# Performance work log

Hardware: AMD Instinct MI355X
Metric: run time of the kernel (lower is better)

The kernel has to match this reference:

```python
import jax, jax.numpy as jnp
import numpy as np

DIM = 256  # channel width
B, H, W = 4, 64, 64


def conv2d(x, w, b, pad, groups=1):
    # x: NCHW, w: OIHW (I = C_in/groups)
    y = jax.lax.conv_general_dilated(
        x, w, window_strides=(1, 1),
        padding=[(pad[0], pad[0]), (pad[1], pad[1])],
        dimension_numbers=("NCHW", "OIHW", "NCHW"),
        feature_group_count=groups)
    return y + b[None, :, None, None]


def l2norm(x, eps=1e-12):
    # matches F.normalize(x, dim=-1): x / max(||x||_2, eps)
    n = jnp.sqrt(jnp.sum(x * x, axis=-1, keepdims=True))
    return x / jnp.maximum(n, eps)


def setup_inputs() -> dict:
    key = jax.random.key(0)
    ks = jax.random.split(key, 12)
    dim, c8 = DIM, DIM // 8
    w = lambda k, shape, s: jax.random.normal(k, shape, jnp.float32) * s
    return {
        "x": jax.random.normal(ks[0], (B, dim, H, W), jnp.float32),
        "w_conv": w(ks[1], (dim, dim, 3, 3), 0.02), "b_conv": jnp.zeros((dim,), jnp.float32),
        "w01": w(ks[2], (dim, 1, 1, 7), 0.05), "b01": jnp.zeros((dim,), jnp.float32),
        "w02": w(ks[3], (dim, 1, 7, 1), 0.05), "b02": jnp.zeros((dim,), jnp.float32),
        "w11": w(ks[4], (dim, 1, 1, 11), 0.05), "b11": jnp.zeros((dim,), jnp.float32),
        "w12": w(ks[5], (dim, 1, 11, 1), 0.05), "b12": jnp.zeros((dim,), jnp.float32),
        "w21": w(ks[6], (dim, 1, 1, 21), 0.05), "b21": jnp.zeros((dim,), jnp.float32),
        "w22": w(ks[7], (dim, 1, 21, 1), 0.05), "b22": jnp.zeros((dim,), jnp.float32),
        "w_proj": w(ks[8], (c8, dim, 1, 1), 0.05), "b_proj": jnp.zeros((c8,), jnp.float32),
        "w3": w(ks[9], (c8, dim // 4, 1, 1), 0.05), "b3": jnp.zeros((c8,), jnp.float32),
        "w4": w(ks[10], (dim, c8, 1, 1), 0.05), "b4": jnp.zeros((dim,), jnp.float32),
    }


def reference(x, w_conv, b_conv, w01, b01, w02, b02, w11, b11, w12, b12,
              w21, b21, w22, b22, w_proj, b_proj, w3, b3, w4, b4):
    b, c, h, w_ = x.shape
    x = conv2d(x, w_conv, b_conv, (1, 1))
    # multi-scale separable depthwise convs (7, 11, 21)
    x1 = conv2d(conv2d(x, w01, b01, (0, 3), c), w02, b02, (3, 0), c)
    x2 = conv2d(conv2d(x, w11, b11, (0, 5), c), w12, b12, (5, 0), c)
    x3 = conv2d(conv2d(x, w21, b21, (0, 10), c), w22, b22, (10, 0), c)
    out1 = x1 + x2 + x3 + x                      # [b, dim, h, w]
    out1 = conv2d(out1, w_proj, b_proj, (0, 0))  # [b, dim//8, h, w]
    c8 = out1.shape[1]
    t = out1.reshape(b, c8, h * w_)              # b head c (h w), head=1

    q1 = l2norm(t)
    attn1 = jax.nn.softmax(q1 @ jnp.swapaxes(q1, -2, -1), axis=-1)  # [b, c8, c8]
    out2 = attn1 @ t                                                # [b, c8, hw]

    # branch 2: spatial attention (hw x hw)
    ts = jnp.swapaxes(t, -2, -1)                 # [b, hw, c8]
    q2 = l2norm(ts)
    attn2 = jax.nn.softmax(q2 @ jnp.swapaxes(q2, -2, -1), axis=-1)  # [b, hw, hw]
    out3 = jnp.swapaxes(attn2 @ ts, -2, -1)                         # [b, c8, hw]

    out4 = jnp.concatenate([out2.reshape(b, c8, h, w_),
                            out3.reshape(b, c8, h, w_)], axis=1)    # [b, dim//4, h, w]
    out5 = conv2d(out4, w3, b3, (0, 0)) + out1
    return conv2d(out5, w4, b4, (0, 0))          # [b, dim, h, w]
```

## Files before the change

### kernel.cpp

```cpp
#include <hip/hip_runtime.h>
#include <hip/hip_bf16.h>

typedef __hip_bfloat16 bf16;
typedef short s16;
typedef __attribute__((ext_vector_type(4))) short s16x4;
typedef __attribute__((ext_vector_type(8))) short s16x8;
typedef __attribute__((ext_vector_type(4))) float f32x4;

__device__ __forceinline__ s16 f2b(float f){
    unsigned u = __float_as_uint(f);
    unsigned r = (u + 0x7FFFu + ((u >> 16) & 1u)) >> 16;
    return (s16)r;
}
__device__ __forceinline__ float b2f_bits(s16 v){
    return __uint_as_float(((unsigned)(unsigned short)v) << 16);
}

__global__ __launch_bounds__(256) void xtrans_k(const float* __restrict__ x, s16* __restrict__ xcl){
    __shared__ s16 lb[64][258];
    int h = blockIdx.x, b = blockIdx.y, t = threadIdx.x;
    for (int i = t; i < 16384; i += 256){
        int ci = i >> 6, w = i & 63;
        lb[w][ci] = f2b(x[((b*256 + ci)*64 + h)*64 + w]);
    }
    __syncthreads();
    for (int i = t; i < 16384; i += 256){
        int w = i >> 8, ci = i & 255;
        xcl[(b*4096 + h*64 + w)*256 + ci] = lb[w][ci];
    }
}

__global__ __launch_bounds__(256) void wpack_k(const float* __restrict__ w, s16* __restrict__ wpk){
    int idx = blockIdx.x*256 + threadIdx.x;
    int cil = idx & 31;
    int r   = idx >> 5;
    int co  = r & 255;
    int r2  = r >> 8;
    int tap = r2 % 9, cc = r2 / 9;
    wpk[idx] = f2b(w[(co*256 + cc*32 + cil)*9 + tap]);
}

__global__ __launch_bounds__(256) void conv3x3m_k(const s16* __restrict__ xcl,
        const s16* __restrict__ wpk, const float* __restrict__ bias,
        bf16* __restrict__ y0){
    __shared__ alignas(16) s16 smem[30240];
    s16* xls = smem;
    s16* wls = smem + 9504;
    const int sp = blockIdx.x, cog = blockIdx.y;
    const int b = sp >> 5, h0 = (sp & 31)*2;
    const int t = threadIdx.x;
    const int wv = t >> 6, lane = t & 63;
    const int lm = lane & 15, g = lane >> 4;

    f32x4 acc[2][4];
    #pragma unroll
    for (int mi = 0; mi < 2; ++mi)
        #pragma unroll
        for (int ni = 0; ni < 4; ++ni) acc[mi][ni] = (f32x4){0.f,0.f,0.f,0.f};

    for (int cc = 0; cc < 8; ++cc){
        __syncthreads();
        for (int i = t; i < 1056; i += 256){
            int g8 = i & 3, wi = (i>>2) % 66, r = (i>>2) / 66;
            int h = h0 - 1 + r, w = wi - 1;
            s16x8 v = {0,0,0,0,0,0,0,0};
            if (h >= 0 && h < 64 && w >= 0 && w < 64)
                v = *(const s16x8*)&xcl[(b*4096 + h*64 + w)*256 + cc*32 + g8*8];
            s16* d = &xls[(r*66 + wi)*36 + g8*8];
            *(s16x4*)d       = __builtin_shufflevector(v, v, 0,1,2,3);
            *(s16x4*)(d + 4) = __builtin_shufflevector(v, v, 4,5,6,7);
        }
        for (int i = t; i < 2304; i += 256){
            int g8 = i & 3, co = (i>>2) & 63, tap = i >> 8;
            s16x8 v = *(const s16x8*)&wpk[((cc*9 + tap)*256 + cog*64 + co)*32 + g8*8];
            s16* d = &wls[(tap*64 + co)*36 + g8*8];
            *(s16x4*)d       = __builtin_shufflevector(v, v, 0,1,2,3);
            *(s16x4*)(d + 4) = __builtin_shufflevector(v, v, 4,5,6,7);
        }
        __syncthreads();
        #pragma unroll
        for (int tap = 0; tap < 9; ++tap){
            const int kh = tap/3, kw = tap%3;
            s16x8 bfr[4], afr[2];
            #pragma unroll
            for (int ni = 0; ni < 4; ++ni){
                const s16* p = &wls[(tap*64 + ni*16 + lm)*36 + g*8];
                s16x4 lo = *(const s16x4*)p;
                s16x4 hi = *(const s16x4*)(p + 4);
                bfr[ni] = __builtin_shufflevector(lo, hi, 0,1,2,3,4,5,6,7);
            }
            #pragma unroll
            for (int mi = 0; mi < 2; ++mi){
                int m = (wv*2 + mi)*16 + lm;
                int hr = m >> 6, ww = m & 63;
                const s16* p = &xls[((hr + kh)*66 + (ww + kw))*36 + g*8];
                s16x4 lo = *(const s16x4*)p;
                s16x4 hi = *(const s16x4*)(p + 4);
                afr[mi] = __builtin_shufflevector(lo, hi, 0,1,2,3,4,5,6,7);
            }
            #pragma unroll
            for (int mi = 0; mi < 2; ++mi)
                #pragma unroll
                for (int ni = 0; ni < 4; ++ni)
                    acc[mi][ni] = __builtin_amdgcn_mfma_f32_16x16x32_bf16(
                        afr[mi], bfr[ni], acc[mi][ni], 0, 0, 0);
        }
    }
    __syncthreads();
    float* ot = (float*)smem;
    #pragma unroll
    for (int mi = 0; mi < 2; ++mi)
        #pragma unroll
        for (int ni = 0; ni < 4; ++ni)
            #pragma unroll
            for (int r = 0; r < 4; ++r){
                int m  = (wv*2 + mi)*16 + g*4 + r;
                int co = ni*16 + lm;
                ot[co*132 + m] = acc[mi][ni][r];
            }
    __syncthreads();
    for (int i = t; i < 8192; i += 256){
        int co = i >> 7, m = i & 127;
        float v = ot[co*132 + m] + bias[cog*64 + co];
        y0[((b*256 + cog*64 + co)*64 + h0 + (m>>6))*64 + (m & 63)] = __float2bfloat16(v);
    }
}

template<int K>
__device__ __forceinline__ void sep_branch(const float (*__restrict__ pl)[65], float (*__restrict__ hp)[65],
                                           int c, int t,
                                           const float* __restrict__ wh, const float* __restrict__ bh,
                                           const float* __restrict__ wv, const float* __restrict__ bv,
                                           float* acc){
    constexpr int P = K/2;
    constexpr int W = 16 + 2*P;
    float wk[K];
    #pragma unroll
    for (int j = 0; j < K; ++j) wk[j] = wh[c*K + j];
    float bhv = bh[c];
    {
        int h = t >> 2, w0 = (t & 3)*16;
        float win[W];
        #pragma unroll
        for (int j = 0; j < W; ++j){
            int ww = w0 - P + j;
            win[j] = (ww >= 0 && ww < 64) ? pl[h][ww] : 0.f;
        }
        __syncthreads();
        #pragma unroll
        for (int i = 0; i < 16; ++i){
            float s = bhv;
            #pragma unroll
            for (int k = 0; k < K; ++k) s += win[i+k]*wk[k];
            hp[h][w0 + i] = s;
        }
    }
    float vk[K];
    #pragma unroll
    for (int j = 0; j < K; ++j) vk[j] = wv[c*K + j];
    float bvv = bv[c];
    __syncthreads();
    {
        int w = t & 63, h0 = (t >> 6)*16;
        float win[W];
        #pragma unroll
        for (int j = 0; j < W; ++j){
            int hh = h0 - P + j;
            win[j] = (hh >= 0 && hh < 64) ? hp[hh][w] : 0.f;
        }
        #pragma unroll
        for (int i = 0; i < 16; ++i){
            float s = bvv;
            #pragma unroll
            for (int k = 0; k < K; ++k) s += win[i+k]*vk[k];
            acc[i] += s;
        }
    }
}

__global__ __launch_bounds__(256) void sepconv_k(const bf16* __restrict__ y0,
        const float* __restrict__ w01, const float* __restrict__ b01,
        const float* __restrict__ w02, const float* __restrict__ b02,
        const float* __restrict__ w11, const float* __restrict__ b11,
        const float* __restrict__ w12, const float* __restrict__ b12,
        const float* __restrict__ w21, const float* __restrict__ b21,
        const float* __restrict__ w22, const float* __restrict__ b22,
        bf16* __restrict__ out1){
    __shared__ float pl[64][65];
    __shared__ float hp[64][65];
    int bc = blockIdx.x;
    int c = bc & 255;
    int t = threadIdx.x;
    const bf16* src = y0 + bc*4096;
    for (int i = t; i < 4096; i += 256) pl[i>>6][i&63] = __bfloat162float(src[i]);
    __syncthreads();
    float acc[16];
    #pragma unroll
    for (int k = 0; k < 16; ++k) acc[k] = 0.f;
    sep_branch<7 >(pl, hp, c, t, w01, b01, w02, b02, acc);
    sep_branch<11>(pl, hp, c, t, w11, b11, w12, b12, acc);
    sep_branch<21>(pl, hp, c, t, w21, b21, w22, b22, acc);
    bf16* dst = out1 + bc*4096;
    {
        int w = t & 63, h0 = (t >> 6)*16;
        #pragma unroll
        for (int i = 0; i < 16; ++i)
            dst[(h0 + i)*64 + w] = __float2bfloat16(acc[i] + pl[h0 + i][w]);
    }
}

__global__ __launch_bounds__(256) void proj_k(const bf16* __restrict__ out1, const float* __restrict__ wp,
                                              const float* __restrict__ bp, float* __restrict__ tbuf,
                                              s16* __restrict__ tTb, float* __restrict__ rn2){
    __shared__ float wl[256*32];
    __shared__ s16 part[4][64][36];
    int pt = blockIdx.x, b = blockIdx.y, t = threadIdx.x;
    int q = t >> 6, lane = t & 63;
    for (int i = t; i < 8192; i += 256){
        int ci = i >> 5, cc = i & 31;
        wl[ci*32 + cc] = wp[cc*256 + ci];
    }
    __syncthreads();
    int p = pt*64 + lane;
    float acc[32] = {};
    const bf16* xb = out1 + b*1048576 + p;
    for (int ci = q*64; ci < q*64 + 64; ++ci){
        float v = __bfloat162float(xb[ci*4096]);
        const float* wr = &wl[ci*32];
        #pragma unroll
        for (int c8 = 0; c8 < 8; ++c8){
            float4 w4 = *(const float4*)&wr[c8*4];
            acc[c8*4+0] += w4.x*v; acc[c8*4+1] += w4.y*v;
            acc[c8*4+2] += w4.z*v; acc[c8*4+3] += w4.w*v;
        }
    }
    #pragma unroll
    for (int cc = 0; cc < 32; ++cc) part[q][lane][cc] = f2b(acc[cc]);
    __syncthreads();
    int p_loc = t >> 2, qq = t & 3;
    int pg = pt*64 + p_loc;
    float a8[8];
    float ss = 0.f;
    #pragma unroll
    for (int c = 0; c < 8; ++c){
        int cc = qq*8 + c;
        float v = b2f_bits(part[0][p_loc][cc]) + b2f_bits(part[1][p_loc][cc])
                + b2f_bits(part[2][p_loc][cc]) + b2f_bits(part[3][p_loc][cc]) + bp[cc];
        a8[c] = v;
        ss += v*v;
    }
    ss += __shfl_xor(ss, 1, 4);
    ss += __shfl_xor(ss, 2, 4);
    if (qq == 0) rn2[b*4096 + pg] = 1.f / fmaxf(sqrtf(ss), 1e-12f);
    #pragma unroll
    for (int c = 0; c < 8; ++c) tbuf[(b*32 + qq*8 + c)*4096 + pg] = a8[c];
    s16x8 o8;
    #pragma unroll
    for (int c = 0; c < 8; ++c) o8[c] = f2b(a8[c]);
    *(s16x8*)&tTb[(b*4096 + pg)*32 + qq*8] = o8;
}

__global__ __launch_bounds__(256) void gramm_k(const float* __restrict__ tbuf, float* __restrict__ part){
    __shared__ alignas(16) s16 ts[32*268];
    int ks = blockIdx.x, b = blockIdx.y, t = threadIdx.x;
    {
        int cc = t >> 3, p0 = (t & 7)*32;
        const float* src = tbuf + (b*32 + cc)*4096 + ks*256 + p0;
        s16* d = &ts[cc*268 + p0];
        #pragma unroll
        for (int q = 0; q < 4; ++q){
            float4 v0 = *(const float4*)&src[q*8];
            float4 v1 = *(const float4*)&src[q*8 + 4];
            s16x4 o0, o1;
            o0[0]=f2b(v0.x); o0[1]=f2b(v0.y); o0[2]=f2b(v0.z); o0[3]=f2b(v0.w);
            o1[0]=f2b(v1.x); o1[1]=f2b(v1.y); o1[2]=f2b(v1.z); o1[3]=f2b(v1.w);
            *(s16x4*)&d[q*8]     = o0;
            *(s16x4*)&d[q*8 + 4] = o1;
        }
    }
    __syncthreads();
    int wv = t >> 6, lane = t & 63, lm = lane & 15, g = lane >> 4;
    int mi = wv >> 1, ni = wv & 1;
    f32x4 acc = (f32x4){0.f,0.f,0.f,0.f};
    const s16* ar = &ts[(mi*16 + lm)*268];
    const s16* br = &ts[(ni*16 + lm)*268];
    #pragma unroll
    for (int kk = 0; kk < 8; ++kk){
        const s16* ap = ar + kk*32 + g*8;
        s16x4 alo = *(const s16x4*)ap;
        s16x4 ahi = *(const s16x4*)(ap + 4);
        s16x8 af = __builtin_shufflevector(alo, ahi, 0,1,2,3,4,5,6,7);
        const s16* bp = br + kk*32 + g*8;
        s16x4 blo = *(const s16x4*)bp;
        s16x4 bhi = *(const s16x4*)(bp + 4);
        s16x8 bf = __builtin_shufflevector(blo, bhi, 0,1,2,3,4,5,6,7);
        acc = __builtin_amdgcn_mfma_f32_16x16x32_bf16(af, bf, acc, 0, 0, 0);
    }
    float* pd = part + (b*16 + ks)*1024;
    #pragma unroll
    for (int r = 0; r < 4; ++r){
        int i = mi*16 + g*4 + r, j = ni*16 + lm;
        pd[i*32 + j] = acc[r];
    }
}

__global__ __launch_bounds__(64) void attn1_k(const float* __restrict__ part,
                                              float* __restrict__ attn1T){
    int i = blockIdx.x, b = blockIdx.y, j = threadIdx.x;
    float gij = 0.f, gjj = 0.f;
    if (j < 32){
        #pragma unroll 8
        for (int ps = 0; ps < 16; ++ps){
            const float* pp = part + (b*16+ps)*1024;
            gij += pp[i*32 + j];
            gjj += pp[j*33];
        }
    }
    float rnj = 1.f / fmaxf(sqrtf(gjj), 1e-12f);
    float rni = __shfl(rnj, i, 64);
    float e = (j < 32) ? __expf(rni*rnj*gij) : 0.f;
    float sum = e;
    #pragma unroll
    for (int o = 32; o > 0; o >>= 1) sum += __shfl_xor(sum, o, 64);
    if (j < 32) attn1T[b*1024 + j*32 + i] = e / sum;
}

__global__ __launch_bounds__(256) void fold_k(const float* __restrict__ attn1T,
        const float* __restrict__ w3, const float* __restrict__ b3,
        const float* __restrict__ w4, const float* __restrict__ b4,
        float* __restrict__ WtT, float* __restrict__ WoT, float* __restrict__ bfo){
    __shared__ float a1[1024];
    __shared__ float w3a[1024];
    __shared__ float w3bs[1024];
    int b = blockIdx.x, t = threadIdx.x;
    for (int idx = t; idx < 1024; idx += 256){
        int i = idx >> 5, j = idx & 31;
        a1[idx]   = attn1T[b*1024 + j*32 + i];
        w3bs[idx] = w3[i*64 + 32 + j];
    }
    __syncthreads();
    for (int idx = t; idx < 1024; idx += 256){
        int cc = idx >> 5, j = idx & 31;
        float s = 0.f;
        #pragma unroll 8
        for (int i = 0; i < 32; ++i) s += w3[cc*64 + i]*a1[i*32 + j];
        w3a[idx] = s;
    }
    __syncthreads();
    int co = t;
    float w4r[32];
    #pragma unroll
    for (int cc = 0; cc < 32; ++cc) w4r[cc] = w4[co*32 + cc];
    float bfv = b4[co];
    #pragma unroll
    for (int cc = 0; cc < 32; ++cc) bfv += w4r[cc]*b3[cc];
    bfo[b*256 + co] = bfv;
    for (int j = 0; j < 32; ++j){
        float st = w4r[j];
        float so = 0.f;
        #pragma unroll 8
        for (int cc = 0; cc < 32; ++cc){
            st += w4r[cc]*w3a[cc*32 + j];
            so += w4r[cc]*w3bs[cc*32 + j];
        }
        WtT[(b*32 + j)*256 + co] = st;
        WoT[(b*32 + j)*256 + co] = so;
    }
}

__global__ __launch_bounds__(256) void flashm_k(const s16* __restrict__ tTb, const float* __restrict__ rn2,
                                                float* __restrict__ partA, float* __restrict__ partL){
    __shared__ alignas(16) s16 kvb[128*36];
    __shared__ alignas(16) s16 vts[32*132];
    __shared__ alignas(16) s16 pls[4][16*132];
    __shared__ float rnj[128];
    __shared__ float ri[64];
    const int ib = blockIdx.x, b = blockIdx.y, chunk = blockIdx.z;
    const int t = threadIdx.x, wv = t >> 6, lane = t & 63;
    const int lm = lane & 15, g = lane >> 4;
    const int i0 = ib*64;

    if (t < 64) ri[t] = rn2[b*4096 + i0 + t];
    s16x8 qf = *(const s16x8*)&tTb[(b*4096 + i0 + wv*16 + lm)*32 + g*8];
    __syncthreads();
    float rni4[4];
    #pragma unroll
    for (int r = 0; r < 4; ++r) rni4[r] = ri[wv*16 + g*4 + r];

    f32x4 oacc[2];
    oacc[0] = (f32x4){0.f,0.f,0.f,0.f};
    oacc[1] = (f32x4){0.f,0.f,0.f,0.f};
    float lacc[4] = {0.f,0.f,0.f,0.f};
    s16* pw = pls[wv];

    for (int jt = chunk*8; jt < chunk*8 + 8; ++jt){
        const int j0 = jt*128;
        __syncthreads();
        for (int gi = t; gi < 512; gi += 256){
            int j = gi >> 2, g8 = gi & 3;
            s16x8 v = *(const s16x8*)&tTb[(b*4096 + j0 + j)*32 + g8*8];
            s16* d = &kvb[j*36 + g8*8];
            *(s16x4*)d       = __builtin_shufflevector(v, v, 0,1,2,3);
            *(s16x4*)(d + 4) = __builtin_shufflevector(v, v, 4,5,6,7);
            #pragma unroll
            for (int e = 0; e < 8; ++e) vts[(g8*8 + e)*132 + j] = v[e];
        }
        if (t < 128) rnj[t] = rn2[b*4096 + j0 + t];
        __syncthreads();
        #pragma unroll
        for (int nt = 0; nt < 8; ++nt){
            const s16* bp = &kvb[(nt*16 + lm)*36 + g*8];
            s16x4 blo = *(const s16x4*)bp;
            s16x4 bhi = *(const s16x4*)(bp + 4);
            s16x8 bf = __builtin_shufflevector(blo, bhi, 0,1,2,3,4,5,6,7);
            f32x4 s = __builtin_amdgcn_mfma_f32_16x16x32_bf16(qf, bf,
                        (f32x4){0.f,0.f,0.f,0.f}, 0, 0, 0);
            float rj = rnj[nt*16 + lm];
            #pragma unroll
            for (int r = 0; r < 4; ++r){
                float e = __expf(s[r]*rni4[r]*rj);
                lacc[r] += e;
                pw[(g*4 + r)*132 + nt*16 + lm] = f2b(e);
            }
        }
        #pragma unroll
        for (int ks = 0; ks < 4; ++ks){
            const s16* ap = &pw[lm*132 + ks*32 + g*8];
            s16x4 alo = *(const s16x4*)ap;
            s16x4 ahi = *(const s16x4*)(ap + 4);
            s16x8 af = __builtin_shufflevector(alo, ahi, 0,1,2,3,4,5,6,7);
            #pragma unroll
            for (int n2 = 0; n2 < 2; ++n2){
                const s16* vp = &vts[(n2*16 + lm)*132 + ks*32 + g*8];
                s16x4 vlo = *(const s16x4*)vp;
                s16x4 vhi = *(const s16x4*)(vp + 4);
                s16x8 vf = __builtin_shufflevector(vlo, vhi, 0,1,2,3,4,5,6,7);
                oacc[n2] = __builtin_amdgcn_mfma_f32_16x16x32_bf16(af, vf, oacc[n2], 0, 0, 0);
            }
        }
    }
    #pragma unroll
    for (int r = 0; r < 4; ++r){
        float v = lacc[r];
        v += __shfl_xor(v, 1, 16); v += __shfl_xor(v, 2, 16);
        v += __shfl_xor(v, 4, 16); v += __shfl_xor(v, 8, 16);
        lacc[r] = v;
    }
    const int base = (b*4 + chunk)*4096 + i0 + wv*16;
    #pragma unroll
    for (int n2 = 0; n2 < 2; ++n2)
        #pragma unroll
        for (int r = 0; r < 4; ++r)
            partA[(base + g*4 + r)*32 + n2*16 + lm] = oacc[n2][r];
    if (lm == 0){
        #pragma unroll
        for (int r = 0; r < 4; ++r) partL[base + g*4 + r] = lacc[r];
    }
}

__global__ __launch_bounds__(256) void finalfuse_k(const float* __restrict__ tbuf,
        const float* __restrict__ partA, const float* __restrict__ partL,
        const float* __restrict__ WtT, const float* __restrict__ WoT,
        const float* __restrict__ bfo, float* __restrict__ out){
    int pt = blockIdx.x, cog = blockIdx.y, b = blockIdx.z, t = threadIdx.x;
    int p = pt*256 + t;
    float l = 0.f;
    #pragma unroll
    for (int c = 0; c < 4; ++c) l += partL[(b*4 + c)*4096 + p];
    float inv = 1.f / l;
    float v3[32];
    #pragma unroll
    for (int q = 0; q < 8; ++q){
        float4 s0 = *(const float4*)&partA[((b*4 + 0)*4096 + p)*32 + q*4];
        float4 s1 = *(const float4*)&partA[((b*4 + 1)*4096 + p)*32 + q*4];
        float4 s2 = *(const float4*)&partA[((b*4 + 2)*4096 + p)*32 + q*4];
        float4 s3 = *(const float4*)&partA[((b*4 + 3)*4096 + p)*32 + q*4];
        v3[q*4+0] = (s0.x + s1.x + s2.x + s3.x)*inv;
        v3[q*4+1] = (s0.y + s1.y + s2.y + s3.y)*inv;
        v3[q*4+2] = (s0.z + s1.z + s2.z + s3.z)*inv;
        v3[q*4+3] = (s0.w + s1.w + s2.w + s3.w)*inv;
    }
    float acc[32];
    #pragma unroll
    for (int co = 0; co < 32; ++co) acc[co] = bfo[b*256 + cog*32 + co];
    for (int j = 0; j < 32; ++j){
        float vt = tbuf[(b*32 + j)*4096 + p];
        float vo = v3[j];
        const float* wtr = WtT + (b*32 + j)*256 + cog*32;
        const float* wor = WoT + (b*32 + j)*256 + cog*32;
        #pragma unroll
        for (int co = 0; co < 32; ++co) acc[co] += wtr[co]*vt + wor[co]*vo;
    }
    #pragma unroll
    for (int co = 0; co < 32; ++co)
        out[((b*256 + cog*32 + co)*4096) + p] = acc[co];
}

extern "C" void kernel_launch(void* const* d_in, const int* in_sizes, int n_in,
                              void* d_out, int out_size, void* d_ws, size_t ws_size,
                              hipStream_t stream) {
    const float* x      = (const float*)d_in[0];
    const float* w_conv = (const float*)d_in[1];
    const float* b_conv = (const float*)d_in[2];
    const float* w01 = (const float*)d_in[3];  const float* b01 = (const float*)d_in[4];
    const float* w02 = (const float*)d_in[5];  const float* b02 = (const float*)d_in[6];
    const float* w11 = (const float*)d_in[7];  const float* b11 = (const float*)d_in[8];
    const float* w12 = (const float*)d_in[9];  const float* b12 = (const float*)d_in[10];
    const float* w21 = (const float*)d_in[11]; const float* b21 = (const float*)d_in[12];
    const float* w22 = (const float*)d_in[13]; const float* b22 = (const float*)d_in[14];
    const float* w_proj = (const float*)d_in[15]; const float* b_proj = (const float*)d_in[16];
    const float* w3 = (const float*)d_in[17]; const float* b3 = (const float*)d_in[18];
    const float* w4 = (const float*)d_in[19]; const float* b4 = (const float*)d_in[20];

    char* wsb = (char*)d_ws;
    s16*   xcl  = (s16*)wsb;
    bf16*  out1 = (bf16*)wsb;
    bf16*  y0   = (bf16*)(wsb + 8388608);
    s16*   wpk  = (s16*)(wsb + 16777216);
    float* f    = (float*)d_ws;
    float* part   = f + 0;
    float* partA  = f + 0;
    float* tbuf   = f + 2097152;
    s16*   tTb    = (s16*)(wsb + 10485760);
    float* WtT    = f + 3145728;
    float* WoT    = f + 3178496;
    float* bfo    = f + 3211264;
    float* partL  = f + 4194304;
    float* attn1T = f + 4722816;
    float* rn2    = f + 4726912;

    xtrans_k<<<dim3(64, 4), 256, 0, stream>>>(x, xcl);
    wpack_k<<<dim3(2304), 256, 0, stream>>>(w_conv, wpk);
    conv3x3m_k<<<dim3(128, 4), 256, 0, stream>>>(xcl, wpk, b_conv, y0);
    sepconv_k<<<dim3(1024), 256, 0, stream>>>(y0, w01, b01, w02, b02,
                                              w11, b11, w12, b12,
                                              w21, b21, w22, b22, out1);
    proj_k<<<dim3(64, 4), 256, 0, stream>>>(out1, w_proj, b_proj, tbuf, tTb, rn2);
    gramm_k<<<dim3(16, 4), 256, 0, stream>>>(tbuf, part);
    attn1_k<<<dim3(32, 4), 64, 0, stream>>>(part, attn1T);
    fold_k<<<dim3(4), 256, 0, stream>>>(attn1T, w3, b3, w4, b4, WtT, WoT, bfo);
    flashm_k<<<dim3(64, 4, 4), 256, 0, stream>>>(tTb, rn2, partA, partL);
    finalfuse_k<<<dim3(16, 8, 4), 256, 0, stream>>>(tbuf, partA, partL, WtT, WoT, bfo,
                                                    (float*)d_out);
}
```

Baseline: 308.5 us.

## Merge prep kernels, fold attn1 into afold, drop fp32 tbuf for bf16 tTb

```diff
diff --git a/kernel.cpp b/kernel.cpp
--- a/kernel.cpp
+++ b/kernel.cpp
@@ -16,28 +16,34 @@
     return __uint_as_float(((unsigned)(unsigned short)v) << 16);
 }
 
-__global__ __launch_bounds__(256) void xtrans_k(const float* __restrict__ x, s16* __restrict__ xcl){
+__global__ __launch_bounds__(256) void prep_k(const float* __restrict__ x, s16* __restrict__ xcl,
+                                              const float* __restrict__ w, s16* __restrict__ wpk){
     __shared__ s16 lb[64][258];
-    int h = blockIdx.x, b = blockIdx.y, t = threadIdx.x;
-    for (int i = t; i < 16384; i += 256){
-        int ci = i >> 6, w = i & 63;
-        lb[w][ci] = f2b(x[((b*256 + ci)*64 + h)*64 + w]);
-    }
-    __syncthreads();
-    for (int i = t; i < 16384; i += 256){
-        int w = i >> 8, ci = i & 255;
-        xcl[(b*4096 + h*64 + w)*256 + ci] = lb[w][ci];
-    }
-}
-
-__global__ __launch_bounds__(256) void wpack_k(const float* __restrict__ w, s16* __restrict__ wpk){
-    int idx = blockIdx.x*256 + threadIdx.x;
-    int cil = idx & 31;
-    int r   = idx >> 5;
-    int co  = r & 255;
-    int r2  = r >> 8;
-    int tap = r2 % 9, cc = r2 / 9;
-    wpk[idx] = f2b(w[(co*256 + cc*32 + cil)*9 + tap]);
+    int blk = blockIdx.x, t = threadIdx.x;
+    if (blk < 256){
+        int h = blk & 63, b = blk >> 6;
+        for (int i = t; i < 16384; i += 256){
+            int ci = i >> 6, ww = i & 63;
+            lb[ww][ci] = f2b(x[((b*256 + ci)*64 + h)*64 + ww]);
+        }
+        __syncthreads();
+        for (int i = t; i < 16384; i += 256){
+            int ww = i >> 8, ci = i & 255;
+            xcl[(b*4096 + h*64 + ww)*256 + ci] = lb[ww][ci];
+        }
+    } else {
+        int base = (blk - 256)*1024 + t;
+        #pragma unroll
+        for (int k = 0; k < 4; ++k){
+            int idx = base + k*256;
+            int cil = idx & 31;
+            int r   = idx >> 5;
+            int co  = r & 255;
+            int r2  = r >> 8;
+            int tap = r2 % 9, cc = r2 / 9;
+            wpk[idx] = f2b(w[(co*256 + cc*32 + cil)*9 + tap]);
+        }
+    }
 }
 
 __global__ __launch_bounds__(256) void conv3x3m_k(const s16* __restrict__ xcl,
@@ -210,7 +216,7 @@
 }
 
 __global__ __launch_bounds__(256) void proj_k(const bf16* __restrict__ out1, const float* __restrict__ wp,
-                                              const float* __restrict__ bp, float* __restrict__ tbuf,
+                                              const float* __restrict__ bp,
                                               s16* __restrict__ tTb, float* __restrict__ rn2){
     __shared__ float wl[256*32];
     __shared__ s16 part[4][64][36];
@@ -252,31 +258,26 @@
     ss += __shfl_xor(ss, 1, 4);
     ss += __shfl_xor(ss, 2, 4);
     if (qq == 0) rn2[b*4096 + pg] = 1.f / fmaxf(sqrtf(ss), 1e-12f);
-    #pragma unroll
-    for (int c = 0; c < 8; ++c) tbuf[(b*32 + qq*8 + c)*4096 + pg] = a8[c];
     s16x8 o8;
     #pragma unroll
     for (int c = 0; c < 8; ++c) o8[c] = f2b(a8[c]);
     *(s16x8*)&tTb[(b*4096 + pg)*32 + qq*8] = o8;
 }
 
-__global__ __launch_bounds__(256) void gramm_k(const float* __restrict__ tbuf, float* __restrict__ part){
+__global__ __launch_bounds__(256) void gramm_k(const s16* __restrict__ tTb, float* __restrict__ part){
     __shared__ alignas(16) s16 ts[32*268];
     int ks = blockIdx.x, b = blockIdx.y, t = threadIdx.x;
     {
-        int cc = t >> 3, p0 = (t & 7)*32;
-        const float* src = tbuf + (b*32 + cc)*4096 + ks*256 + p0;
-        s16* d = &ts[cc*268 + p0];
+        const s16* src = &tTb[(b*4096 + ks*256 + t)*32];
+        s16 row[32];
         #pragma unroll
         for (int q = 0; q < 4; ++q){
-            float4 v0 = *(const float4*)&src[q*8];
-            float4 v1 = *(const float4*)&src[q*8 + 4];
-            s16x4 o0, o1;
-            o0[0]=f2b(v0.x); o0[1]=f2b(v0.y); o0[2]=f2b(v0.z); o0[3]=f2b(v0.w);
-            o1[0]=f2b(v1.x); o1[1]=f2b(v1.y); o1[2]=f2b(v1.z); o1[3]=f2b(v1.w);
-            *(s16x4*)&d[q*8]     = o0;
-            *(s16x4*)&d[q*8 + 4] = o1;
-        }
+            s16x8 v = *(const s16x8*)&src[q*8];
+            #pragma unroll
+            for (int e = 0; e < 8; ++e) row[q*8 + e] = v[e];
+        }
+        #pragma unroll
+        for (int cc = 0; cc < 32; ++cc) ts[cc*268 + t] = row[cc];
     }
     __syncthreads();
     int wv = t >> 6, lane = t & 63, lm = lane & 15, g = lane >> 4;
@@ -304,40 +305,43 @@
     }
 }
 
-__global__ __launch_bounds__(64) void attn1_k(const float* __restrict__ part,
-                                              float* __restrict__ attn1T){
-    int i = blockIdx.x, b = blockIdx.y, j = threadIdx.x;
-    float gij = 0.f, gjj = 0.f;
-    if (j < 32){
-        #pragma unroll 8
-        for (int ps = 0; ps < 16; ++ps){
-            const float* pp = part + (b*16+ps)*1024;
-            gij += pp[i*32 + j];
-            gjj += pp[j*33];
-        }
-    }
-    float rnj = 1.f / fmaxf(sqrtf(gjj), 1e-12f);
-    float rni = __shfl(rnj, i, 64);
-    float e = (j < 32) ? __expf(rni*rnj*gij) : 0.f;
-    float sum = e;
-    #pragma unroll
-    for (int o = 32; o > 0; o >>= 1) sum += __shfl_xor(sum, o, 64);
-    if (j < 32) attn1T[b*1024 + j*32 + i] = e / sum;
-}
-
-__global__ __launch_bounds__(256) void fold_k(const float* __restrict__ attn1T,
+__global__ __launch_bounds__(256) void afold_k(const float* __restrict__ part,
         const float* __restrict__ w3, const float* __restrict__ b3,
         const float* __restrict__ w4, const float* __restrict__ b4,
         float* __restrict__ WtT, float* __restrict__ WoT, float* __restrict__ bfo){
+    __shared__ float rn[32];
+    __shared__ float rsum[32];
     __shared__ float a1[1024];
     __shared__ float w3a[1024];
     __shared__ float w3bs[1024];
     int b = blockIdx.x, t = threadIdx.x;
+    if (t < 32){
+        float gjj = 0.f;
+        #pragma unroll 8
+        for (int ps = 0; ps < 16; ++ps) gjj += part[(b*16+ps)*1024 + t*33];
+        rn[t] = 1.f / fmaxf(sqrtf(gjj), 1e-12f);
+    }
     for (int idx = t; idx < 1024; idx += 256){
         int i = idx >> 5, j = idx & 31;
-        a1[idx]   = attn1T[b*1024 + j*32 + i];
         w3bs[idx] = w3[i*64 + 32 + j];
     }
+    __syncthreads();
+    for (int e = t; e < 1024; e += 256){
+        int i = e >> 5, j = e & 31;
+        float gij = 0.f;
+        #pragma unroll 8
+        for (int ps = 0; ps < 16; ++ps) gij += part[(b*16+ps)*1024 + e];
+        a1[e] = __expf(rn[i]*rn[j]*gij);
+    }
+    __syncthreads();
+    if (t < 32){
+        float s = 0.f;
+        #pragma unroll 8
+        for (int j = 0; j < 32; ++j) s += a1[t*32 + j];
+        rsum[t] = 1.f / s;
+    }
+    __syncthreads();
+    for (int e = t; e < 1024; e += 256) a1[e] *= rsum[e >> 5];
     __syncthreads();
     for (int idx = t; idx < 1024; idx += 256){
         int cc = idx >> 5, j = idx & 31;
@@ -458,7 +462,7 @@
     }
 }
 
-__global__ __launch_bounds__(256) void finalfuse_k(const float* __restrict__ tbuf,
+__global__ __launch_bounds__(256) void finalfuse_k(const s16* __restrict__ tTb,
         const float* __restrict__ partA, const float* __restrict__ partL,
         const float* __restrict__ WtT, const float* __restrict__ WoT,
         const float* __restrict__ bfo, float* __restrict__ out){
@@ -480,16 +484,26 @@
         v3[q*4+2] = (s0.z + s1.z + s2.z + s3.z)*inv;
         v3[q*4+3] = (s0.w + s1.w + s2.w + s3.w)*inv;
     }
+    float vt[32];
+    {
+        const s16* tp = &tTb[(b*4096 + p)*32];
+        #pragma unroll
+        for (int q = 0; q < 4; ++q){
+            s16x8 v = *(const s16x8*)&tp[q*8];
+            #pragma unroll
+            for (int e = 0; e < 8; ++e) vt[q*8 + e] = b2f_bits(v[e]);
+        }
+    }
     float acc[32];
     #pragma unroll
     for (int co = 0; co < 32; ++co) acc[co] = bfo[b*256 + cog*32 + co];
     for (int j = 0; j < 32; ++j){
-        float vt = tbuf[(b*32 + j)*4096 + p];
-        float vo = v3[j];
+        float vtj = vt[j];
+        float vo  = v3[j];
         const float* wtr = WtT + (b*32 + j)*256 + cog*32;
         const float* wor = WoT + (b*32 + j)*256 + cog*32;
         #pragma unroll
-        for (int co = 0; co < 32; ++co) acc[co] += wtr[co]*vt + wor[co]*vo;
+        for (int co = 0; co < 32; ++co) acc[co] += wtr[co]*vtj + wor[co]*vo;
     }
     #pragma unroll
     for (int co = 0; co < 32; ++co)
@@ -520,26 +534,22 @@
     float* f    = (float*)d_ws;
     float* part   = f + 0;
     float* partA  = f + 0;
-    float* tbuf   = f + 2097152;
     s16*   tTb    = (s16*)(wsb + 10485760);
     float* WtT    = f + 3145728;
     float* WoT    = f + 3178496;
     float* bfo    = f + 3211264;
     float* partL  = f + 4194304;
-    float* attn1T = f + 4722816;
     float* rn2    = f + 4726912;
 
-    xtrans_k<<<dim3(64, 4), 256, 0, stream>>>(x, xcl);
-    wpack_k<<<dim3(2304), 256, 0, stream>>>(w_conv, wpk);
+    prep_k<<<dim3(832), 256, 0, stream>>>(x, xcl, w_conv, wpk);
     conv3x3m_k<<<dim3(128, 4), 256, 0, stream>>>(xcl, wpk, b_conv, y0);
     sepconv_k<<<dim3(1024), 256, 0, stream>>>(y0, w01, b01, w02, b02,
                                               w11, b11, w12, b12,
                                               w21, b21, w22, b22, out1);
-    proj_k<<<dim3(64, 4), 256, 0, stream>>>(out1, w_proj, b_proj, tbuf, tTb, rn2);
-    gramm_k<<<dim3(16, 4), 256, 0, stream>>>(tbuf, part);
-    attn1_k<<<dim3(32, 4), 64, 0, stream>>>(part, attn1T);
-    fold_k<<<dim3(4), 256, 0, stream>>>(attn1T, w3, b3, w4, b4, WtT, WoT, bfo);
+    proj_k<<<dim3(64, 4), 256, 0, stream>>>(out1, w_proj, b_proj, tTb, rn2);
+    gramm_k<<<dim3(16, 4), 256, 0, stream>>>(tTb, part);
+    afold_k<<<dim3(4), 256, 0, stream>>>(part, w3, b3, w4, b4, WtT, WoT, bfo);
     flashm_k<<<dim3(64, 4, 4), 256, 0, stream>>>(tTb, rn2, partA, partL);
-    finalfuse_k<<<dim3(16, 8, 4), 256, 0, stream>>>(tbuf, partA, partL, WtT, WoT, bfo,
+    finalfuse_k<<<dim3(16, 8, 4), 256, 0, stream>>>(tTb, partA, partL, WtT, WoT, bfo,
                                                     (float*)d_out);
 }
```

New measurement: 294.7 us. 1.05x faster.
